# Kernel optimization log

Hardware: AMD Instinct MI355X
Metric: run time of the kernel (lower is better)

Reference implementation:

```python
import jax, jax.numpy as jnp
import numpy as np

EPS = 1e-15  # matches torch_geometric.nn.dense.dmon_pool.EPS


def setup_inputs() -> dict:
    key = jax.random.key(0)
    k1, k2, k3, k4 = jax.random.split(key, 4)
    B, N, C, K = 8, 4096, 128, 64
    x = jax.random.normal(k1, (B, N, C), dtype=jnp.float32)
    adj = jax.random.uniform(k2, (B, N, N), dtype=jnp.float32)
    # Linear(C -> K) params of the cluster-assignment MLP
    weight = jax.random.normal(k3, (C, K), dtype=jnp.float32) / np.sqrt(C)
    bias = jax.random.normal(k4, (K,), dtype=jnp.float32) * 0.01
    return {"x": x, "adj": adj, "weight": weight, "bias": bias}


def reference(x, adj, weight, bias):
    B, N, C = x.shape
    K = weight.shape[1]
    dt = x.dtype

    # cluster assignment: linear + softmax (dropout = 0)
    s = jax.nn.softmax(x @ weight + bias, axis=-1)            # [B, N, K]

    # pooled features: selu(S^T X)
    out = jax.nn.selu(jnp.einsum('bnk,bnc->bkc', s, x))       # [B, K, C]

    # pooled adjacency: S^T A S
    sT_adj = jnp.einsum('bnk,bnm->bkm', s, adj)               # [B, K, N]
    out_adj = jnp.einsum('bkm,bml->bkl', sT_adj, s)           # [B, K, K]

    # spectral (modularity) loss
    deg = adj.sum(-1)                                         # [B, N]
    m = deg.sum(-1) / 2                                       # [B]
    ca = jnp.einsum('bnk,bn->bk', s, deg)                     # [B, K] (== cb)
    normalizer = ca[:, :, None] * ca[:, None, :] / 2 / m[:, None, None]
    decompose = out_adj - normalizer
    spectral_loss = (-jnp.trace(decompose, axis1=-2, axis2=-1) / 2 / m).mean()

    # orthogonality loss
    ss = jnp.einsum('bnk,bnl->bkl', s, s)                     # [B, K, K]
    ss_fro = jnp.linalg.norm(ss, axis=(-2, -1), keepdims=True)
    i_s = jnp.eye(K, dtype=dt)
    sqrt_k = jnp.sqrt(jnp.asarray(K, dt))
    ortho_loss = jnp.linalg.norm(ss / ss_fro - i_s / sqrt_k, axis=(-2, -1)).mean()

    # cluster-size loss (mask = all-ones, so mask.sum == N)
    cluster_size = s.sum(axis=1)                              # [B, K]
    cluster_loss = (jnp.linalg.norm(cluster_size, axis=1) / N * sqrt_k - 1).mean()

    # zero the diagonal, then symmetric degree-normalize the pooled adjacency
    out_adj = out_adj * (1.0 - i_s)
    d = jnp.sqrt(out_adj.sum(-1)) + EPS                       # [B, K]
    out_adj = out_adj / d[:, None, :] / d[:, :, None]

    return s, out, out_adj, spectral_loss, ortho_loss, cluster_loss
```

## Files before the change

### kernel.cpp

```cpp
#include <hip/hip_runtime.h>
#include <hip/hip_bf16.h>


typedef _Float16 f16x8 __attribute__((ext_vector_type(8)));
typedef float f32x4 __attribute__((ext_vector_type(4)));

#define MFMA16(a, b, c) __builtin_amdgcn_mfma_f32_16x16x32_f16((a), (b), (c), 0, 0, 0)

__device__ __forceinline__ void gld_lds16(const void* g, void* l) {
  __builtin_amdgcn_global_load_lds(
      (const __attribute__((address_space(1))) void*)g,
      (__attribute__((address_space(3))) void*)l, 16, 0, 0);
}

template <int NCHUNK>
__device__ __forceinline__ void stage_lds(const void* g, void* lbase, int tid) {
  char* ld = (char*)lbase + (tid >> 6) * 1024;
  const char* gs = (const char*)g + tid * 16;
#pragma unroll
  for (int p = 0; p < NCHUNK; ++p)
    gld_lds16(gs + p * 4096, ld + p * 4096);
}

__global__ __launch_bounds__(256) void k_assign(
    const float* __restrict__ x, const float* __restrict__ w,
    const float* __restrict__ bias, float* __restrict__ s_out,
    _Float16* __restrict__ sB) {
  __shared__ __align__(16) _Float16 wT[2][64][136];
  __shared__ __align__(16) float sT[64][76];
  const int b = blockIdx.x & 7;
  const int it = blockIdx.x >> 3;
  const int n_base = it * 64;
  const int tid = threadIdx.x;

  for (int idx = tid; idx < 8192; idx += 256) {
    int c = idx >> 6, k = idx & 63;
    float v = w[idx];
    _Float16 h = (_Float16)v;
    wT[0][k][c] = h;
    wT[1][k][c] = (_Float16)(v - (float)h);
  }
  const int l = tid & 63, wv = tid >> 6;
  const int l15 = l & 15, g = l >> 4;
  float bv[4];
#pragma unroll
  for (int ct = 0; ct < 4; ++ct) bv[ct] = bias[ct * 16 + l15];
  __syncthreads();

  f32x4 acc[4];
#pragma unroll
  for (int ct = 0; ct < 4; ++ct) acc[ct] = (f32x4){bv[ct], bv[ct], bv[ct], bv[ct]};

  const float* xrow = x + ((size_t)(b * 4096 + n_base + wv * 16 + l15)) * 128;
#pragma unroll
  for (int cs = 0; cs < 4; ++cs) {
    const int c0 = cs * 32;
    f32x4 r0 = *(const f32x4*)(xrow + c0 + 8 * g);
    f32x4 r1 = *(const f32x4*)(xrow + c0 + 8 * g + 4);
    f16x8 ah, al;
#pragma unroll
    for (int j = 0; j < 4; ++j) {
      float v0 = r0[j]; _Float16 h0 = (_Float16)v0;
      ah[j] = h0; al[j] = (_Float16)(v0 - (float)h0);
      float v1 = r1[j]; _Float16 h1 = (_Float16)v1;
      ah[4 + j] = h1; al[4 + j] = (_Float16)(v1 - (float)h1);
    }
#pragma unroll
    for (int ct = 0; ct < 4; ++ct) {
      f16x8 bh = *(const f16x8*)&wT[0][ct * 16 + l15][c0 + 8 * g];
      f16x8 bl = *(const f16x8*)&wT[1][ct * 16 + l15][c0 + 8 * g];
      acc[ct] = MFMA16(ah, bh, acc[ct]);
      acc[ct] = MFMA16(al, bh, acc[ct]);
      acc[ct] = MFMA16(ah, bl, acc[ct]);
    }
  }

#pragma unroll
  for (int r = 0; r < 4; ++r) {
    float m = fmaxf(fmaxf(acc[0][r], acc[1][r]), fmaxf(acc[2][r], acc[3][r]));
#pragma unroll
    for (int off = 1; off < 16; off <<= 1) m = fmaxf(m, __shfl_xor(m, off, 64));
    float e[4], sum = 0.f;
#pragma unroll
    for (int ct = 0; ct < 4; ++ct) { e[ct] = __expf(acc[ct][r] - m); sum += e[ct]; }
#pragma unroll
    for (int off = 1; off < 16; off <<= 1) sum += __shfl_xor(sum, off, 64);
    float inv = 1.0f / sum;
#pragma unroll
    for (int ct = 0; ct < 4; ++ct) acc[ct][r] = e[ct] * inv;
  }

  const int row_l = wv * 16 + 4 * g;
  float* srow = s_out + ((size_t)(b * 4096 + n_base)) * 64;
#pragma unroll
  for (int r = 0; r < 4; ++r)
#pragma unroll
    for (int ct = 0; ct < 4; ++ct) {
      srow[(size_t)(row_l + r) * 64 + ct * 16 + l15] = acc[ct][r];
      sT[ct * 16 + l15][row_l + r] = acc[ct][r];
    }
  __syncthreads();

  _Float16* dst = sB + (size_t)(b * 64 + it) * 4096;
#pragma unroll
  for (int p = 0; p < 2; ++p) {
    int slot = tid + 256 * p;
    int ks = slot >> 8, ct = (slot >> 6) & 3, ln = slot & 63;
    int col = ct * 16 + (ln & 15);
    int row0 = ks * 32 + 8 * (ln >> 4);
    f16x8 o;
#pragma unroll
    for (int j = 0; j < 8; ++j) o[j] = (_Float16)sT[col][row0 + j];
    *(f16x8*)(dst + slot * 8) = o;
  }
}

__global__ __launch_bounds__(512, 4) void k_fused(
    const float* __restrict__ adj, const _Float16* __restrict__ sB,
    const float* __restrict__ s_out, const float* __restrict__ x,
    float* __restrict__ oadj_part, float* __restrict__ ss_part,
    float* __restrict__ p_part, float* __restrict__ csp) {
  __shared__ __align__(16) char pool[73728];
  const int tid = threadIdx.x;

  if (blockIdx.x < 512) {
    const int b = blockIdx.x & 7;
    const int nt = blockIdx.x >> 3;
    const int n_base = nt * 64;
    const int l = tid & 63, w = tid >> 6;
    const int rt = w & 3, ch = w >> 2;
    const int g = l >> 4;

    const char* sBb = (const char*)(sB + (size_t)b * 64 * 4096);
    const char* asrc = (const char*)adj +
        ((size_t)(b * 4096 + n_base + (tid >> 4)) * 4096) * 4 +
        (((tid & 15) * 16) ^ (((tid >> 4) & 7) << 4));
    const size_t CH1 = (size_t)32 * 16384;
    const char* fsrc = sBb + tid * 16;

    auto stage = [&](int s, int buf) {
      char* ab = pool + buf * 16384 + w * 1024;
      const char* a0 = asrc + (size_t)s * 256;
      gld_lds16(a0, ab);
      gld_lds16(a0 + CH1, ab + 8192);
      gld_lds16(fsrc + (size_t)s * 8192, pool + 49152 + buf * 8192 + w * 1024);
    };

    stage(0, 0);
    stage(1, 1);

    const int rowbase = (rt * 16 + (l & 15)) * 256;
    const int swz = (l & 7) << 4;
    int innerX[4];
#pragma unroll
    for (int ks = 0; ks < 2; ++ks)
#pragma unroll
      for (int part = 0; part < 2; ++part)
        innerX[ks * 2 + part] = (ks * 128 + g * 32 + part * 16) ^ swz;

    f32x4 acc[2] = {};
    int buf = 0;
    for (int s = 0; s < 64; ++s) {
      if (s == 63) asm volatile("s_waitcnt vmcnt(0)" ::: "memory");
      else         asm volatile("s_waitcnt vmcnt(3)" ::: "memory");
      __builtin_amdgcn_sched_barrier(0);
      __builtin_amdgcn_s_barrier();
      if (s < 62) {
        int nb = buf + 2; if (nb >= 3) nb -= 3;
        stage(s + 2, nb);
      }
      const char* ab = pool + buf * 16384;
      const char* fbb = pool + 49152 + buf * 8192;
#pragma unroll
      for (int ks = 0; ks < 2; ++ks) {
        f32x4 lo = *(const f32x4*)(ab + rowbase + innerX[ks * 2]);
        f32x4 hi = *(const f32x4*)(ab + rowbase + innerX[ks * 2 + 1]);
        f16x8 af;
#pragma unroll
        for (int j = 0; j < 4; ++j) {
          af[j] = (_Float16)lo[j];
          af[4 + j] = (_Float16)hi[j];
        }
        f16x8 b0 = *(const f16x8*)(fbb + (ks * 4 + ch * 2 + 0) * 1024 + l * 16);
        f16x8 b1 = *(const f16x8*)(fbb + (ks * 4 + ch * 2 + 1) * 1024 + l * 16);
        acc[0] = MFMA16(af, b0, acc[0]);
        acc[1] = MFMA16(af, b1, acc[1]);
      }
      buf = (buf == 2) ? 0 : buf + 1;
    }

    {
      const char* ssrc =
          (const char*)(s_out + (size_t)(b * 4096 + n_base) * 64) + tid * 16;
      gld_lds16(ssrc, pool + 16384 + w * 1024);
      gld_lds16(ssrc + 8192, pool + 16384 + w * 1024 + 8192);
    }
    __syncthreads();

    float* Yl = (float*)pool;
    float* sl = (float*)(pool + 16384);
#pragma unroll
    for (int c2 = 0; c2 < 2; ++c2) {
      const int ct = ch * 2 + c2;
#pragma unroll
      for (int r = 0; r < 4; ++r)
        Yl[(rt * 16 + (l >> 4) * 4 + r) * 64 + ct * 16 + (l & 15)] = acc[c2][r];
    }
    __syncthreads();

    const int kq = tid >> 4, lq = tid & 15;
    f32x4 a2a = {}, a2b = {};
    for (int r = 0; r < 64; ++r) {
      float sA = sl[r * 64 + kq];
      float sC = sl[r * 64 + 32 + kq];
      f32x4 y4 = *(const f32x4*)(Yl + r * 64 + lq * 4);
#pragma unroll
      for (int j = 0; j < 4; ++j) { a2a[j] += sA * y4[j]; a2b[j] += sC * y4[j]; }
    }
    float* op = oadj_part + ((size_t)(b * 64 + nt)) * 4096;
    *(f32x4*)(op + kq * 64 + lq * 4) = a2a;
    *(f32x4*)(op + (kq + 32) * 64 + lq * 4) = a2b;
  } else {
    const int bid2 = blockIdx.x - 512;
    const int b = bid2 & 7;
    const int ch = bid2 >> 3;
    const bool act = tid < 256;
    float* sc = (float*)pool;
    float* xc = (float*)(pool + 8192);
    float* qc = (float*)(pool + 8192 + 16384);
    const int kq = tid >> 4, cq = tid & 15;
    const int kk = tid & 63, nq = tid >> 6;
    f32x4 ssa[4] = {};
    f32x4 pa[8] = {};
    float csA = 0.f;
    for (int sub = 0; sub < 8; ++sub) {
      if (sub) __syncthreads();
      const int nb = ch * 256 + sub * 32;
      if (act) {
        stage_lds<2>(s_out + ((size_t)(b * 4096 + nb)) * 64, sc, tid);
        stage_lds<4>(x + ((size_t)(b * 4096 + nb)) * 128, xc, tid);
      }
      __syncthreads();
      if (act) {
        for (int n = 0; n < 32; ++n) {
          f32x4 s4 = *(const f32x4*)(sc + n * 64 + kq * 4);
          f32x4 s4b = *(const f32x4*)(sc + n * 64 + cq * 4);
          f32x4 x4a = *(const f32x4*)(xc + n * 128 + cq * 8);
          f32x4 x4b = *(const f32x4*)(xc + n * 128 + cq * 8 + 4);
#pragma unroll
          for (int i = 0; i < 4; ++i) {
#pragma unroll
            for (int j = 0; j < 4; ++j) {
              ssa[i][j] += s4[i] * s4b[j];
              pa[i * 2][j] += s4[i] * x4a[j];
              pa[i * 2 + 1][j] += s4[i] * x4b[j];
            }
          }
        }
        for (int n = nq; n < 32; n += 4) csA += sc[n * 64 + kk];
      }
    }
    if (act) {
      float* sp = ss_part + ((size_t)(b * 16 + ch)) * 4096;
      float* pp = p_part + ((size_t)(b * 16 + ch)) * 8192;
#pragma unroll
      for (int i = 0; i < 4; ++i) {
        *(f32x4*)(sp + (kq * 4 + i) * 64 + cq * 4) = ssa[i];
        *(f32x4*)(pp + (kq * 4 + i) * 128 + cq * 8) = pa[i * 2];
        *(f32x4*)(pp + (kq * 4 + i) * 128 + cq * 8 + 4) = pa[i * 2 + 1];
      }
    }
    __syncthreads();
    if (act) { qc[nq * 64 + kk] = csA; }
    __syncthreads();
    if (tid < 64)
      csp[(size_t)(b * 16 + ch) * 64 + tid] =
          qc[0 * 64 + tid] + qc[1 * 64 + tid] + qc[2 * 64 + tid] + qc[3 * 64 + tid];
  }
}

__global__ __launch_bounds__(256) void k_reduce(
    const float* __restrict__ oadj_part, const float* __restrict__ ss_part,
    const float* __restrict__ p_part, float* __restrict__ oadj_raw,
    float* __restrict__ ss_sum, float* __restrict__ out_feat) {
  const int gid = blockIdx.x * 256 + threadIdx.x;
  if (gid < 32768) {
    int b = gid >> 12, e = gid & 4095;
    float s = 0.f;
    for (int t = 0; t < 64; ++t) s += oadj_part[((size_t)(b * 64 + t)) * 4096 + e];
    oadj_raw[gid] = s;
  } else if (gid < 65536) {
    int g2 = gid - 32768, b = g2 >> 12, e = g2 & 4095;
    float s = 0.f;
    for (int t = 0; t < 16; ++t) s += ss_part[((size_t)(b * 16 + t)) * 4096 + e];
    ss_sum[g2] = s;
  } else {
    int g3 = gid - 65536, b = g3 >> 13, e = g3 & 8191;
    float s = 0.f;
    for (int t = 0; t < 16; ++t) s += p_part[((size_t)(b * 16 + t)) * 8192 + e];
    const float scale = 1.0507009873554805f, alpha = 1.6732632423543772f;
    out_feat[g3] = s > 0.f ? scale * s : scale * alpha * (expf(s) - 1.f);
  }
}

__global__ __launch_bounds__(256) void k_finalize(
    const float* __restrict__ oadj_raw, const float* __restrict__ ss_sum,
    const float* __restrict__ csp, float* __restrict__ out_adj,
    float* __restrict__ loss_part) {
  __shared__ float red[256];
  __shared__ float ca[64], dvec[64], diag[64];
  const int b = blockIdx.x, t = threadIdx.x;
  const float* ob = oadj_raw + b * 4096;
  const float* ssb = ss_sum + b * 4096;

  if (t < 64) {
    const float* orow = ob + t * 64;
    float full = 0.f, nod = 0.f;
    for (int lc = 0; lc < 64; ++lc) {
      float v = orow[lc];
      full += v;
      nod += (lc != t) ? v : 0.f;
    }
    ca[t] = full;
    dvec[t] = sqrtf(nod) + 1e-15f;
    diag[t] = orow[t];
  }
  __syncthreads();

  red[t] = (t < 64) ? ca[t] : 0.f;
  __syncthreads();
  for (int o = 128; o > 0; o >>= 1) { if (t < o) red[t] += red[t + o]; __syncthreads(); }
  const float sm = red[0];
  __syncthreads();

  red[t] = (t < 64) ? (diag[t] - ca[t] * ca[t] / sm) : 0.f;
  __syncthreads();
  for (int o = 128; o > 0; o >>= 1) { if (t < o) red[t] += red[t + o]; __syncthreads(); }
  const float spectral_b = -red[0] / sm;
  __syncthreads();

  float fp = 0.f;
  for (int i = t; i < 4096; i += 256) { float v = ssb[i]; fp += v * v; }
  red[t] = fp; __syncthreads();
  for (int o = 128; o > 0; o >>= 1) { if (t < o) red[t] += red[t + o]; __syncthreads(); }
  const float fro = sqrtf(red[0]);
  __syncthreads();
  float op2 = 0.f;
  for (int i = t; i < 4096; i += 256) {
    float v = ssb[i] / fro - (((i >> 6) == (i & 63)) ? 0.125f : 0.f);
    op2 += v * v;
  }
  red[t] = op2; __syncthreads();
  for (int o = 128; o > 0; o >>= 1) { if (t < o) red[t] += red[t + o]; __syncthreads(); }
  const float ortho_b = sqrtf(red[0]);
  __syncthreads();

  float csize_k = 0.f;
  if (t < 64) {
    for (int ch = 0; ch < 16; ++ch) csize_k += csp[(size_t)(b * 16 + ch) * 64 + t];
  }
  red[t] = (t < 64) ? csize_k * csize_k : 0.f;
  __syncthreads();
  for (int o = 128; o > 0; o >>= 1) { if (t < o) red[t] += red[t + o]; __syncthreads(); }
  const float cluster_b = sqrtf(red[0]) * 8.f / 4096.f - 1.f;
  __syncthreads();

  for (int i = t; i < 4096; i += 256) {
    int kk = i >> 6, lc = i & 63;
    float v = (kk == lc) ? 0.f : ob[i] / (dvec[kk] * dvec[lc]);
    out_adj[(size_t)b * 4096 + i] = v;
  }
  if (t == 0) {
    loss_part[b * 3 + 0] = spectral_b;
    loss_part[b * 3 + 1] = ortho_b;
    loss_part[b * 3 + 2] = cluster_b;
  }
}

__global__ void k_scalars(const float* __restrict__ lp, float* __restrict__ o3) {
  if (threadIdx.x == 0) {
    float s = 0.f, o = 0.f, c = 0.f;
    for (int b = 0; b < 8; ++b) { s += lp[b * 3]; o += lp[b * 3 + 1]; c += lp[b * 3 + 2]; }
    o3[0] = s * 0.125f; o3[1] = o * 0.125f; o3[2] = c * 0.125f;
  }
}

extern "C" void kernel_launch(void* const* d_in, const int* in_sizes, int n_in,
                              void* d_out, int out_size, void* d_ws, size_t ws_size,
                              hipStream_t stream) {
  const float* x = (const float*)d_in[0];
  const float* adj = (const float*)d_in[1];
  const float* w = (const float*)d_in[2];
  const float* bias = (const float*)d_in[3];
  float* out = (float*)d_out;
  float* s_out = out;
  float* out_feat = out + 2097152;
  float* out_adj = out + 2162688;
  float* out_sc = out + 2195456;

  char* ws = (char*)d_ws;
  _Float16* sB = (_Float16*)ws;
  float* oadj_part = (float*)(ws + (8u << 20));
  float* ss_part = (float*)(ws + (16u << 20));
  float* p_part = (float*)(ws + (20u << 20));
  float* oadj_raw = (float*)(ws + (28u << 20) + (128u << 10));
  float* ss_sum = (float*)(ws + (28u << 20) + (256u << 10));
  float* loss_part = (float*)(ws + (28u << 20) + (384u << 10));
  float* csp = (float*)(ws + (28u << 20) + (512u << 10));

  k_assign<<<dim3(512), dim3(256), 0, stream>>>(x, w, bias, s_out, sB);
  k_fused<<<dim3(640), dim3(512), 0, stream>>>(adj, sB, s_out, x, oadj_part,
                                               ss_part, p_part, csp);
  k_reduce<<<dim3(512), dim3(256), 0, stream>>>(oadj_part, ss_part, p_part,
                                                oadj_raw, ss_sum, out_feat);
  k_finalize<<<dim3(8), dim3(256), 0, stream>>>(oadj_raw, ss_sum, csp,
                                                out_adj, loss_part);
  k_scalars<<<dim3(1), dim3(64), 0, stream>>>(loss_part, out_sc);
}
```

Baseline: 172.2 us.

## Load S fragments straight to registers, shrink LDS and raise occupancy

```diff
diff --git a/kernel.cpp b/kernel.cpp
--- a/kernel.cpp
+++ b/kernel.cpp
@@ -115,12 +115,12 @@
   }
 }
 
-__global__ __launch_bounds__(512, 4) void k_fused(
+__global__ __launch_bounds__(512, 6) void k_fused(
     const float* __restrict__ adj, const _Float16* __restrict__ sB,
     const float* __restrict__ s_out, const float* __restrict__ x,
     float* __restrict__ oadj_part, float* __restrict__ ss_part,
     float* __restrict__ p_part, float* __restrict__ csp) {
-  __shared__ __align__(16) char pool[73728];
+  __shared__ __align__(16) char pool[49152];
   const int tid = threadIdx.x;
 
   if (blockIdx.x < 512) {
@@ -136,18 +136,21 @@
         ((size_t)(b * 4096 + n_base + (tid >> 4)) * 4096) * 4 +
         (((tid & 15) * 16) ^ (((tid >> 4) & 7) << 4));
     const size_t CH1 = (size_t)32 * 16384;
-    const char* fsrc = sBb + tid * 16;
+    const char* fb_lane = sBb + ch * 2048 + l * 16;
 
     auto stage = [&](int s, int buf) {
       char* ab = pool + buf * 16384 + w * 1024;
       const char* a0 = asrc + (size_t)s * 256;
       gld_lds16(a0, ab);
       gld_lds16(a0 + CH1, ab + 8192);
-      gld_lds16(fsrc + (size_t)s * 8192, pool + 49152 + buf * 8192 + w * 1024);
     };
-
-    stage(0, 0);
-    stage(1, 1);
+    auto fragload = [&](int s, f16x8* F) {
+      const char* p = fb_lane + (size_t)s * 8192;
+      F[0] = *(const f16x8*)(p);
+      F[1] = *(const f16x8*)(p + 1024);
+      F[2] = *(const f16x8*)(p + 4096);
+      F[3] = *(const f16x8*)(p + 5120);
+    };
 
     const int rowbase = (rt * 16 + (l & 15)) * 256;
     const int swz = (l & 7) << 4;
@@ -159,18 +162,8 @@
         innerX[ks * 2 + part] = (ks * 128 + g * 32 + part * 16) ^ swz;
 
     f32x4 acc[2] = {};
-    int buf = 0;
-    for (int s = 0; s < 64; ++s) {
-      if (s == 63) asm volatile("s_waitcnt vmcnt(0)" ::: "memory");
-      else         asm volatile("s_waitcnt vmcnt(3)" ::: "memory");
-      __builtin_amdgcn_sched_barrier(0);
-      __builtin_amdgcn_s_barrier();
-      if (s < 62) {
-        int nb = buf + 2; if (nb >= 3) nb -= 3;
-        stage(s + 2, nb);
-      }
+    auto compute = [&](int buf, f16x8* F) {
       const char* ab = pool + buf * 16384;
-      const char* fbb = pool + 49152 + buf * 8192;
 #pragma unroll
       for (int ks = 0; ks < 2; ++ks) {
         f32x4 lo = *(const f32x4*)(ab + rowbase + innerX[ks * 2]);
@@ -181,12 +174,33 @@
           af[j] = (_Float16)lo[j];
           af[4 + j] = (_Float16)hi[j];
         }
-        f16x8 b0 = *(const f16x8*)(fbb + (ks * 4 + ch * 2 + 0) * 1024 + l * 16);
-        f16x8 b1 = *(const f16x8*)(fbb + (ks * 4 + ch * 2 + 1) * 1024 + l * 16);
-        acc[0] = MFMA16(af, b0, acc[0]);
-        acc[1] = MFMA16(af, b1, acc[1]);
+        acc[0] = MFMA16(af, F[ks * 2 + 0], acc[0]);
+        acc[1] = MFMA16(af, F[ks * 2 + 1], acc[1]);
       }
-      buf = (buf == 2) ? 0 : buf + 1;
+    };
+
+    f16x8 Fa[4], Fb[4];
+    stage(0, 0);
+    fragload(0, Fa);
+    stage(1, 1);
+
+    int bufc = 0;
+    for (int s = 0; s < 64; s += 2) {
+      asm volatile("s_waitcnt vmcnt(2)" ::: "memory");
+      __builtin_amdgcn_sched_barrier(0);
+      __builtin_amdgcn_s_barrier();
+      fragload(s + 1, Fb);
+      { int nb = bufc + 2; if (nb >= 3) nb -= 3; if (s + 2 < 64) stage(s + 2, nb); }
+      compute(bufc, Fa);
+      bufc = (bufc == 2) ? 0 : bufc + 1;
+      if (s + 1 == 63) asm volatile("s_waitcnt vmcnt(0)" ::: "memory");
+      else             asm volatile("s_waitcnt vmcnt(2)" ::: "memory");
+      __builtin_amdgcn_sched_barrier(0);
+      __builtin_amdgcn_s_barrier();
+      if (s + 2 < 64) fragload(s + 2, Fa);
+      { int nb = bufc + 2; if (nb >= 3) nb -= 3; if (s + 3 < 64) stage(s + 3, nb); }
+      compute(bufc, Fb);
+      bufc = (bufc == 2) ? 0 : bufc + 1;
     }
 
     {
```

Result: slower. 548.7 us (+218.5%).
